# Optimization experiments

Hardware: AMD Instinct MI355X
Metric: run time of the kernel (lower is better)

The kernel has to match this reference:

```python
import jax, jax.numpy as jnp
import numpy as np

OUT, IN, R = 4096, 4096, 64
B, S = 4, 4096


def setup_inputs() -> dict:
    key = jax.random.key(0)
    ks = jax.random.split(key, 12)
    return {
        "x": jax.random.normal(ks[0], (B, S, IN), dtype=jnp.float32),
        "W": jax.random.normal(ks[1], (OUT, IN), dtype=jnp.float32) * 0.02,
        "bias": jax.random.normal(ks[2], (OUT,), dtype=jnp.float32) * 0.02,
        "U_top": jax.random.normal(ks[3], (OUT, R), dtype=jnp.float32) / np.sqrt(OUT),
        "S_top": jax.random.uniform(ks[4], (R,), dtype=jnp.float32),
        "Vh_top": jax.random.normal(ks[5], (R, IN), dtype=jnp.float32) / np.sqrt(IN),
        "U_tail": jax.random.normal(ks[6], (OUT, R), dtype=jnp.float32) / np.sqrt(OUT),
        "S_tail": jax.random.uniform(ks[7], (R,), dtype=jnp.float32),
        "Vh_tail": jax.random.normal(ks[8], (R, IN), dtype=jnp.float32) / np.sqrt(IN),
        "alpha": jax.random.normal(ks[9], (R,), dtype=jnp.float32) * 0.01,
        "beta": jax.random.normal(ks[10], (R,), dtype=jnp.float32) * 0.01,
        "R": jax.random.normal(ks[11], (R, R), dtype=jnp.float32) * 0.01,
    }


def reference(x, W, bias, U_top, S_top, Vh_top, U_tail, S_tail, Vh_tail, alpha, beta, R):
    # SALT top: gated singular-value correction, relu(S*alpha + beta)
    sigma_top = jax.nn.relu(S_top * alpha + beta)                    # [r]
    W_top_delta = (U_top * sigma_top[None, :]) @ Vh_top              # [out, in]
    # EDoRA tail: B R A with B = U_tail diag(S_tail), A = Vh_tail
    Bm = U_tail * S_tail[None, :]                                    # [out, r]
    delta_tail = Bm @ (R @ Vh_tail)                                  # [out, in]
    W_tilde = W + W_top_delta + delta_tail
    # F.linear: x @ W_tilde.T + bias
    return jnp.einsum('bsi,oi->bso', x, W_tilde) + bias
```

## Files before the change

kernel.cpp:

```cpp
#include <hip/hip_runtime.h>
#include <hip/hip_bf16.h>

#define OUT_DIM 4096
#define IN_DIM  4096
#define RANK    64
#define M_DIM   16384

typedef short  s16x8 __attribute__((ext_vector_type(8)));
typedef __bf16 b16x8 __attribute__((ext_vector_type(8)));
typedef float  f32x4 __attribute__((ext_vector_type(4)));

template <typename T>
__device__ static inline auto mfma_sel(T a, T b, f32x4 c, int)
    -> decltype(__builtin_amdgcn_mfma_f32_16x16x32_bf16(a, b, c, 0, 0, 0)) {
  return __builtin_amdgcn_mfma_f32_16x16x32_bf16(a, b, c, 0, 0, 0);
}
template <typename T>
__device__ static inline f32x4 mfma_sel(T a, T b, f32x4 c, long) {
  return __builtin_amdgcn_mfma_f32_16x16x32_bf16(
      __builtin_bit_cast(b16x8, a), __builtin_bit_cast(b16x8, b), c, 0, 0, 0);
}
__device__ static inline f32x4 mfma_bf16(s16x8 a, s16x8 b, f32x4 c) {
  return mfma_sel(a, b, c, 0);
}

__device__ static inline unsigned short f2bf(float f) {
  unsigned int u = __float_as_uint(f);
  u += 0x7fffu + ((u >> 16) & 1u);
  return (unsigned short)(u >> 16);
}

__device__ static inline void gload16(const unsigned short* g, unsigned short* l) {
  __builtin_amdgcn_global_load_lds(
      (const __attribute__((address_space(1))) void*)g,
      (__attribute__((address_space(3))) void*)l, 16, 0, 0);
}

__global__ void rv2_kernel(const float* __restrict__ Rm, const float* __restrict__ Vh_tail,
                           const float* __restrict__ S_tail, float* __restrict__ RV2) {
  const int i  = blockIdx.x * 256 + threadIdx.x;
  const int r0 = blockIdx.y * 8;
  float acc[8] = {};
  for (int q = 0; q < RANK; ++q) {
    float v = Vh_tail[(size_t)q * IN_DIM + i];
#pragma unroll
    for (int rr = 0; rr < 8; ++rr)
      acc[rr] = fmaf(Rm[(r0 + rr) * RANK + q], v, acc[rr]);
  }
#pragma unroll
  for (int rr = 0; rr < 8; ++rr)
    RV2[(size_t)(r0 + rr) * IN_DIM + i] = acc[rr] * S_tail[r0 + rr];
}

#define CVT_BLOCKS 2048
#define WT_O 16
#define WT_BLOCKS ((IN_DIM / 256) * (OUT_DIM / WT_O))
__global__ void prep_fused_kernel(const float* __restrict__ x, unsigned short* __restrict__ xb,
                                  const float* __restrict__ W,      const float* __restrict__ U_top,
                                  const float* __restrict__ S_top,  const float* __restrict__ alpha,
                                  const float* __restrict__ beta,   const float* __restrict__ U_tail,
                                  const float* __restrict__ Vh_top, const float* __restrict__ RV2,
                                  unsigned short* __restrict__ Wb) {
  const int tid = threadIdx.x;
  if (blockIdx.x < CVT_BLOCKS) {
    const long long n8 = (long long)M_DIM * IN_DIM / 8;
    long long idx = (long long)blockIdx.x * 256 + tid;
    const long long stride = (long long)CVT_BLOCKS * 256;
    for (; idx < n8; idx += stride) {
      const f32x4* p = (const f32x4*)(x + idx * 8);
      f32x4 v0 = p[0], v1 = p[1];
      s16x8 o;
      o[0] = (short)f2bf(v0[0]); o[1] = (short)f2bf(v0[1]);
      o[2] = (short)f2bf(v0[2]); o[3] = (short)f2bf(v0[3]);
      o[4] = (short)f2bf(v1[0]); o[5] = (short)f2bf(v1[1]);
      o[6] = (short)f2bf(v1[2]); o[7] = (short)f2bf(v1[3]);
      *(s16x8*)(xb + idx * 8) = o;
    }
  } else {
    const int rem = blockIdx.x - CVT_BLOCKS;
    const int i   = (rem & 15) * 256 + tid;
    const int o0  = (rem >> 4) * WT_O;
    float acc[WT_O];
#pragma unroll
    for (int o = 0; o < WT_O; ++o) acc[o] = W[(size_t)(o0 + o) * IN_DIM + i];
#pragma unroll 4
    for (int r = 0; r < RANK; ++r) {
      float sig = fmaxf(fmaf(S_top[r], alpha[r], beta[r]), 0.f);
      float vt  = Vh_top[(size_t)r * IN_DIM + i] * sig;
      float rv  = RV2[(size_t)r * IN_DIM + i];
#pragma unroll
      for (int o = 0; o < WT_O; ++o) {
        acc[o] = fmaf(U_top[(o0 + o) * RANK + r],  vt, acc[o]);
        acc[o] = fmaf(U_tail[(o0 + o) * RANK + r], rv, acc[o]);
      }
    }
#pragma unroll
    for (int o = 0; o < WT_O; ++o)
      Wb[(size_t)(o0 + o) * IN_DIM + i] = f2bf(acc[o]);
  }
}

#define BM 256
#define BN 256
#define BK 64
#define NT (IN_DIM / BK)

__global__ __launch_bounds__(512, 2) void gemm_kernel(
    const unsigned short* __restrict__ A,
    const unsigned short* __restrict__ Bw,
    const float* __restrict__ bias,
    float* __restrict__ C) {
  __shared__ unsigned short lds[2][2][BM * BK];

  const int tid = threadIdx.x;
  const int l   = tid & 63;
  const int wid = tid >> 6;
  const int wr  = wid >> 2;
  const int wc  = wid & 3;

  const int bid = blockIdx.x;
  const int swz = (bid & 7) * 128 + (bid >> 3);
  const int nt_ = swz >> 6;
  const int mt_ = swz & 63;
  const long long tileM = (long long)mt_ * BM;
  const long long tileN = (long long)nt_ * BN;

  const int rbase = tid >> 3;
  const int c8    = (((tid & 7) ^ (rbase & 7)) << 3);
  const unsigned short* gA = A  + (tileM + rbase) * (long long)IN_DIM + c8;
  const unsigned short* gB = Bw + (tileN + rbase) * (long long)IN_DIM + c8;

  const int kgrp = l >> 4;
  const int x7   = l & 7;
  const int sc0  = (((0 * 4 + kgrp) ^ x7) << 3);
  const int sc1  = (((1 * 4 + kgrp) ^ x7) << 3);
  const int rba  = (wr * 128 + (l & 15)) * BK;
  const int rbb  = (wc * 64  + (l & 15)) * BK;

  f32x4 acc[8][4] = {};

  {
    unsigned short* la = &lds[0][0][tid * 8];
    unsigned short* lb = &lds[0][1][tid * 8];
#pragma unroll
    for (int j = 0; j < 4; ++j) {
      gload16(gB + (long long)j * 64 * IN_DIM, lb + j * 4096);
      gload16(gA + (long long)j * 64 * IN_DIM, la + j * 4096);
    }
    asm volatile("s_waitcnt vmcnt(0)" ::: "memory");
    asm volatile("s_barrier" ::: "memory");
  }

  int buf = 0;
  for (int t = 0; t < NT; ++t) {
    const long long ktn = (long long)(t + 1) * BK;
    const bool more = (t + 1 < NT);
    const unsigned short* lA = lds[buf][0];
    const unsigned short* lB = lds[buf][1];
    unsigned short* la1 = &lds[buf ^ 1][0][tid * 8];
    unsigned short* lb1 = &lds[buf ^ 1][1][tid * 8];

    s16x8 bfr[4][2];
#pragma unroll
    for (int q = 0; q < 4; ++q) {
      if (q == 0) {
#pragma unroll
        for (int n = 0; n < 4; ++n) {
          bfr[n][0] = *(const s16x8*)&lB[rbb + n * 16 * BK + sc0];
          bfr[n][1] = *(const s16x8*)&lB[rbb + n * 16 * BK + sc1];
        }
      }
      s16x8 afr[2][2];
#pragma unroll
      for (int m2 = 0; m2 < 2; ++m2) {
        afr[m2][0] = *(const s16x8*)&lA[rba + (q * 32 + m2 * 16) * BK + sc0];
        afr[m2][1] = *(const s16x8*)&lA[rba + (q * 32 + m2 * 16) * BK + sc1];
      }

      if (more) {
        if (q == 0) {
          gload16(gB + ktn, lb1);
          gload16(gB + ktn + 1LL * 64 * IN_DIM, lb1 + 4096);
        } else if (q == 1) {
          gload16(gB + ktn + 2LL * 64 * IN_DIM, lb1 + 2 * 4096);
          gload16(gB + ktn + 3LL * 64 * IN_DIM, lb1 + 3 * 4096);
        } else if (q == 2) {
          gload16(gA + ktn, la1);
          gload16(gA + ktn + 2LL * 64 * IN_DIM, la1 + 2 * 4096);
        } else {
          gload16(gA + ktn + 1LL * 64 * IN_DIM, la1 + 1 * 4096);
          gload16(gA + ktn + 3LL * 64 * IN_DIM, la1 + 3 * 4096);
        }
      }

      asm volatile("s_barrier" ::: "memory");

      __builtin_amdgcn_s_setprio(1);
#pragma unroll
      for (int m2 = 0; m2 < 2; ++m2)
#pragma unroll
        for (int n = 0; n < 4; ++n)
#pragma unroll
          for (int kk = 0; kk < 2; ++kk)
            acc[q * 2 + m2][n] = mfma_bf16(afr[m2][kk], bfr[n][kk], acc[q * 2 + m2][n]);
      __builtin_amdgcn_s_setprio(0);

      if (q == 1) {
        if (more) asm volatile("s_waitcnt vmcnt(4)" ::: "memory");
        else      asm volatile("s_waitcnt vmcnt(0)" ::: "memory");
      }
      if (q == 3 && more) {
        asm volatile("s_waitcnt vmcnt(2)" ::: "memory");
      }
      asm volatile("s_barrier" ::: "memory");
    }
    buf ^= 1;
  }

  float bv[4];
#pragma unroll
  for (int n = 0; n < 4; ++n) bv[n] = bias[tileN + wc * 64 + n * 16 + (l & 15)];
#pragma unroll
  for (int m = 0; m < 8; ++m) {
    const long long rbase_c = tileM + wr * 128 + m * 16 + (l >> 4) * 4;
#pragma unroll
    for (int r = 0; r < 4; ++r) {
      float* crow = C + (size_t)(rbase_c + r) * OUT_DIM + tileN + wc * 64 + (l & 15);
#pragma unroll
      for (int n = 0; n < 4; ++n) crow[n * 16] = acc[m][n][r] + bv[n];
    }
  }
}

extern "C" void kernel_launch(void* const* d_in, const int* in_sizes, int n_in,
                              void* d_out, int out_size, void* d_ws, size_t ws_size,
                              hipStream_t stream) {
  const float* x       = (const float*)d_in[0];
  const float* W       = (const float*)d_in[1];
  const float* bias    = (const float*)d_in[2];
  const float* U_top   = (const float*)d_in[3];
  const float* S_top   = (const float*)d_in[4];
  const float* Vh_top  = (const float*)d_in[5];
  const float* U_tail  = (const float*)d_in[6];
  const float* S_tail  = (const float*)d_in[7];
  const float* Vh_tail = (const float*)d_in[8];
  const float* alpha   = (const float*)d_in[9];
  const float* beta    = (const float*)d_in[10];
  const float* Rm      = (const float*)d_in[11];

  char* ws = (char*)d_ws;
  unsigned short* xb  = (unsigned short*)ws;
  unsigned short* Wb  = (unsigned short*)(ws + (size_t)134217728);
  float*          RV2 = (float*)(ws + (size_t)134217728 + 33554432);

  rv2_kernel<<<dim3(IN_DIM / 256, RANK / 8), 256, 0, stream>>>(Rm, Vh_tail, S_tail, RV2);
  prep_fused_kernel<<<CVT_BLOCKS + WT_BLOCKS, 256, 0, stream>>>(
      x, xb, W, U_top, S_top, alpha, beta, U_tail, Vh_top, RV2, Wb);
  gemm_kernel<<<(M_DIM / BM) * (OUT_DIM / BN), 512, 0, stream>>>(xb, Wb, bias,
                                                                 (float*)d_out);
}
```

Baseline: 702.8 us.

## Remap block-to-tile swizzle per XCD and replace asm barriers with builtins

Each XCD's blocks now cover a compact 16x8 rectangle of output tiles instead of a column strip, which is meant to improve L2 reuse of A and B within each XCD. The inline-asm barriers and waitcnts lose their memory clobbers and become s_barrier builtins, with sched_barrier fences placed only after the vmcnt waits. This lets the compiler interleave LDS reads and MFMAs more freely across the barriers. The risk is that dropping the clobbers allows LDS accesses to be reordered past the waits, so correctness now depends on where the sched_barrier fences sit.

```diff
diff --git a/kernel.cpp b/kernel.cpp
--- a/kernel.cpp
+++ b/kernel.cpp
@@ -119,9 +119,10 @@
   const int wc  = wid & 3;
 
   const int bid = blockIdx.x;
-  const int swz = (bid & 7) * 128 + (bid >> 3);
-  const int nt_ = swz >> 6;
-  const int mt_ = swz & 63;
+  const int xcd = bid & 7;
+  const int j   = bid >> 3;
+  const int mt_ = (xcd >> 1) * 16 + (j & 15);
+  const int nt_ = (xcd & 1) * 8 + (j >> 4);
   const long long tileM = (long long)mt_ * BM;
   const long long tileN = (long long)nt_ * BN;
 
@@ -143,12 +144,13 @@
     unsigned short* la = &lds[0][0][tid * 8];
     unsigned short* lb = &lds[0][1][tid * 8];
 #pragma unroll
-    for (int j = 0; j < 4; ++j) {
-      gload16(gB + (long long)j * 64 * IN_DIM, lb + j * 4096);
-      gload16(gA + (long long)j * 64 * IN_DIM, la + j * 4096);
-    }
-    asm volatile("s_waitcnt vmcnt(0)" ::: "memory");
-    asm volatile("s_barrier" ::: "memory");
+    for (int jj = 0; jj < 4; ++jj) {
+      gload16(gB + (long long)jj * 64 * IN_DIM, lb + jj * 4096);
+      gload16(gA + (long long)jj * 64 * IN_DIM, la + jj * 4096);
+    }
+    asm volatile("s_waitcnt vmcnt(0)");
+    __builtin_amdgcn_s_barrier();
+    __builtin_amdgcn_sched_barrier(0);
   }
 
   int buf = 0;
@@ -193,7 +195,7 @@
         }
       }
 
-      asm volatile("s_barrier" ::: "memory");
+      __builtin_amdgcn_s_barrier();
 
       __builtin_amdgcn_s_setprio(1);
 #pragma unroll
@@ -206,13 +208,16 @@
       __builtin_amdgcn_s_setprio(0);
 
       if (q == 1) {
-        if (more) asm volatile("s_waitcnt vmcnt(4)" ::: "memory");
-        else      asm volatile("s_waitcnt vmcnt(0)" ::: "memory");
+        if (more) asm volatile("s_waitcnt vmcnt(4)");
+        else      asm volatile("s_waitcnt vmcnt(0)");
       }
       if (q == 3 && more) {
-        asm volatile("s_waitcnt vmcnt(2)" ::: "memory");
-      }
-      asm volatile("s_barrier" ::: "memory");
+        asm volatile("s_waitcnt vmcnt(2)");
+      }
+      __builtin_amdgcn_s_barrier();
+      if (q == 1 || q == 3) {
+        __builtin_amdgcn_sched_barrier(0);
+      }
     }
     buf ^= 1;
   }
```

After: 697.5 us. Within noise of the previous version (-0.7%).
